# Kernel optimization log

Hardware: AMD Instinct MI355X
Metric: run time of the kernel (lower is better)

The kernel has to match this reference:

```python
import math
import jax, jax.numpy as jnp
import numpy as np

S = 64.0
M = 0.5
C = 1.5
K = 16
EPS = 1e-6
IN = 128
OUT = 10000
B = 1024


def _l2norm(x, axis):
    # matches torch.nn.functional.normalize (eps=1e-12)
    n = jnp.linalg.norm(x, axis=axis, keepdims=True)
    return x / jnp.maximum(n, 1e-12)


def setup_inputs() -> dict:
    key = jax.random.key(0)
    k1, k2, k3, k4 = jax.random.split(key, 4)
    inp = jax.random.normal(k1, (B, IN), dtype=jnp.float32)
    factor = jax.random.uniform(k2, (B, 1), dtype=jnp.float32)
    label = jax.random.randint(k3, (B,), 0, OUT)
    # xavier_uniform over (k, in, out): fan_in=IN, fan_out=OUT (last two dims)
    limit = math.sqrt(6.0 / (IN + OUT))
    weight = jax.random.uniform(k4, (K, IN, OUT), dtype=jnp.float32, minval=-limit, maxval=limit)
    return {"input": inp, "factor": factor, "label": label, "weight": weight}


def reference(input, factor, label, weight):
    # disguise-adaptive margin: (B,1)
    func_a = jnp.power(C, factor / 12.0) * M
    threshold = math.pi - func_a  # (B,1)

    xn = _l2norm(input, axis=1)          # (B, IN)
    wn = _l2norm(weight, axis=1)         # (K, IN, OUT), normalized along IN

    # batched sub-center matmul then max over sub-centers k
    cos_all = jnp.einsum('bf,kfo->kbo', xn, wn)   # (K, B, OUT)
    cos_theta = jnp.max(cos_all, axis=0)          # (B, OUT)

    theta = jnp.arccos(jnp.clip(cos_theta, -1.0 + EPS, 1.0 - EPS))
    one_hot = jax.nn.one_hot(label, OUT, dtype=theta.dtype)  # (B, OUT)
    selected = jnp.where(theta > threshold, jnp.zeros_like(one_hot), one_hot)
    logits = jnp.cos(jnp.where(selected.astype(bool), theta + func_a, theta)) * S

    # cross-entropy (mean reduction)
    logp = jax.nn.log_softmax(logits, axis=-1)
    cls_loss = -jnp.mean(jnp.take_along_axis(logp, label[:, None], axis=1))

    # top-1 accuracy (percent), detached stat
    pred = jnp.argmax(logits, axis=1)
    prec1 = jnp.mean((pred == label).astype(jnp.float32)) * 100.0
    return cls_loss, prec1
```

## Files before the change

kernel.cpp:

```cpp
#include <hip/hip_runtime.h>
#include <hip/hip_bf16.h>
#include <math.h>

#define BB    1024
#define FIN   128
#define NOUT  10000
#define NK    16
#define NBLK  79
#define NPART (NBLK * 2)
#define OPAD  10112
#define LDX   136

typedef __attribute__((ext_vector_type(8))) short short8;
typedef __attribute__((ext_vector_type(4))) float floatx4;

__device__ __forceinline__ unsigned packbf(float a, float b) {
    __hip_bfloat162 h = __float22bfloat162_rn(make_float2(a, b));
    union { __hip_bfloat162 h2; unsigned u; } v;
    v.h2 = h;
    return v.u;
}

__device__ __forceinline__ void async16(const void* g, void* l) {
    __builtin_amdgcn_global_load_lds(
        (const __attribute__((address_space(1))) unsigned int*)g,
        (__attribute__((address_space(3))) unsigned int*)l, 16, 0, 0);
}

__global__ void rowprep(const float* __restrict__ X, const float* __restrict__ factor,
                        float* __restrict__ xinv, float* __restrict__ fa_out,
                        float* __restrict__ thr_out) {
    int b = blockIdx.x;
    int lane = threadIdx.x;
    float v0 = X[b * FIN + lane];
    float v1 = X[b * FIN + 64 + lane];
    float s = v0 * v0 + v1 * v1;
    #pragma unroll
    for (int off = 32; off > 0; off >>= 1) s += __shfl_down(s, off);
    if (lane == 0) {
        float n = sqrtf(s);
        xinv[b] = 1.0f / fmaxf(n, 1e-12f);
        float fa = powf(1.5f, factor[b] * (1.0f / 12.0f)) * 0.5f;
        fa_out[b] = fa;
        thr_out[b] = (float)M_PI - fa;
    }
}

__global__ void wconv(const float* __restrict__ W, unsigned char* __restrict__ Wbf) {
    int t = blockIdx.x * 256 + threadIdx.x;
    int k = t / OPAD;
    int o = t - k * OPAD;
    const bool ok = o < NOUT;
    const float* p = W + (size_t)k * FIN * NOUT + o;
    float v[FIN];
    float s = 0.0f;
    #pragma unroll
    for (int f = 0; f < FIN; f++) {
        float x = ok ? p[(size_t)f * NOUT] : 0.0f;
        v[f] = x;
        s = fmaf(x, x, s);
    }
    float wi = ok ? (1.0f / fmaxf(sqrtf(s), 1e-12f)) : 0.0f;
    unsigned char* dst = Wbf + (size_t)t * 256;
    #pragma unroll
    for (int c = 0; c < 16; c++) {
        uint4 u;
        u.x = packbf(v[c * 8 + 0] * wi, v[c * 8 + 1] * wi);
        u.y = packbf(v[c * 8 + 2] * wi, v[c * 8 + 3] * wi);
        u.z = packbf(v[c * 8 + 4] * wi, v[c * 8 + 5] * wi);
        u.w = packbf(v[c * 8 + 6] * wi, v[c * 8 + 7] * wi);
        *(uint4*)(dst + ((c ^ (o & 15)) * 16)) = u;
    }
}

__global__ __launch_bounds__(256, 2) void gemm_mx(
    const float* __restrict__ X, const unsigned char* __restrict__ Wbf,
    const int* __restrict__ label, const float* __restrict__ xinv,
    float2* __restrict__ partial, float* __restrict__ cosl) {

    __shared__ short lds[32768];

    const int tid  = threadIdx.x;
    const int lane = tid & 63;
    const int w    = tid >> 6;
    const int l15  = lane & 15;
    const int q    = lane >> 4;
    const int wm   = w & 1;
    const int wn   = w >> 1;

    const int id    = blockIdx.x;
    const int group = id >> 6;
    const int sub   = id & 63;
    const int jb    = group * 8 + (sub & 7);
    const int y     = sub >> 3;
    if (jb >= NBLK) return;
    const int r0 = y * 128;
    const int o0 = jb * 128;

    short* xs = lds;
    #pragma unroll
    for (int it = 0; it < 16; it++) {
        int idx = it * 256 + tid;
        int row = idx >> 5;
        int c4  = idx & 31;
        const float4 v = *(const float4*)(X + (size_t)(r0 + row) * FIN + c4 * 4);
        float xi = xinv[r0 + row];
        uint2 p;
        p.x = packbf(v.x * xi, v.y * xi);
        p.y = packbf(v.z * xi, v.w * xi);
        *(uint2*)(xs + row * LDX + c4 * 4) = p;
    }
    __syncthreads();

    short8 af[4][4];
    #pragma unroll
    for (int mt = 0; mt < 4; mt++)
        #pragma unroll
        for (int kk = 0; kk < 4; kk++)
            af[mt][kk] = *(const short8*)(xs + (wm * 64 + mt * 16 + l15) * LDX + kk * 32 + q * 8);
    __syncthreads();

    {
        const unsigned char* g = Wbf + ((size_t)0 * OPAD + o0 + w * 32) * 256 + lane * 16;
        short* d = lds + 0 + w * 4096;
        #pragma unroll
        for (int i = 0; i < 8; i++) async16(g + i * 1024, d + i * 512);
    }

    floatx4 maxv[4][4];
    #pragma unroll
    for (int mt = 0; mt < 4; mt++)
        #pragma unroll
        for (int nt = 0; nt < 4; nt++)
            #pragma unroll
            for (int r = 0; r < 4; r++)
                maxv[mt][nt][r] = -INFINITY;

    for (int k = 0; k < NK; k++) {
        __syncthreads();
        if (k < NK - 1) {
            const unsigned char* g =
                Wbf + ((size_t)(k + 1) * OPAD + o0 + w * 32) * 256 + lane * 16;
            short* d = lds + ((k + 1) & 1) * 16384 + w * 4096;
            #pragma unroll
            for (int i = 0; i < 8; i++) async16(g + i * 1024, d + i * 512);
        }
        const short* wt = lds + (k & 1) * 16384;

        #pragma unroll
        for (int h = 0; h < 2; h++) {
            floatx4 acc[4][2];
            #pragma unroll
            for (int mt = 0; mt < 4; mt++) {
                acc[mt][0] = (floatx4){0.f, 0.f, 0.f, 0.f};
                acc[mt][1] = (floatx4){0.f, 0.f, 0.f, 0.f};
            }
            #pragma unroll
            for (int kk = 0; kk < 4; kk++) {
                short8 bf[2];
                #pragma unroll
                for (int n2 = 0; n2 < 2; n2++) {
                    int col = wn * 64 + (h * 2 + n2) * 16 + l15;
                    int chunk = (kk * 4 + q) ^ l15;
                    bf[n2] = *(const short8*)(wt + col * 128 + chunk * 8);
                }
                #pragma unroll
                for (int mt = 0; mt < 4; mt++) {
                    acc[mt][0] = __builtin_amdgcn_mfma_f32_16x16x32_bf16(af[mt][kk], bf[0], acc[mt][0], 0, 0, 0);
                    acc[mt][1] = __builtin_amdgcn_mfma_f32_16x16x32_bf16(af[mt][kk], bf[1], acc[mt][1], 0, 0, 0);
                }
            }
            #pragma unroll
            for (int mt = 0; mt < 4; mt++)
                #pragma unroll
                for (int n2 = 0; n2 < 2; n2++)
                    #pragma unroll
                    for (int r = 0; r < 4; r++)
                        maxv[mt][h * 2 + n2][r] = fmaxf(maxv[mt][h * 2 + n2][r], acc[mt][n2][r]);
        }
    }

    #pragma unroll
    for (int mt = 0; mt < 4; mt++) {
        #pragma unroll
        for (int rr = 0; rr < 4; rr++) {
            int row = r0 + wm * 64 + mt * 16 + q * 4 + rr;
            int lb = label[row];
            float m = -1e30f, s = 0.f;
            #pragma unroll
            for (int nt = 0; nt < 4; nt++) {
                int o = o0 + wn * 64 + nt * 16 + l15;
                if (o < NOUT) {
                    float c = maxv[mt][nt][rr];
                    if (o == lb) {
                        cosl[row] = c;
                    } else {
                        float l = 64.0f * fminf(fmaxf(c, -1.0f + 1e-6f), 1.0f - 1e-6f);
                        if (l > m) { s = s * __expf(m - l) + 1.0f; m = l; }
                        else       { s += __expf(l - m); }
                    }
                }
            }
            #pragma unroll
            for (int off = 1; off <= 8; off <<= 1) {
                float m2 = __shfl_xor(m, off);
                float s2 = __shfl_xor(s, off);
                float M = fmaxf(m, m2);
                s = s * __expf(m - M) + s2 * __expf(m2 - M);
                m = M;
            }
            if (l15 == 0) partial[(size_t)row * NPART + jb * 2 + wn] = make_float2(m, s);
        }
    }
}

__global__ __launch_bounds__(256, 2) void gemm_stats(
    const float* __restrict__ X, const float* __restrict__ W,
    const int* __restrict__ label, const float* __restrict__ xinv,
    float2* __restrict__ partial, float* __restrict__ cosl) {

    __shared__ short xs[128 * LDX];
    __shared__ short wt[128 * LDX];
    __shared__ float sqs[128][2];

    const int tid  = threadIdx.x;
    const int lane = tid & 63;
    const int w    = tid >> 6;
    const int l15  = lane & 15;
    const int q    = lane >> 4;
    const int wm   = w & 1;
    const int wn   = w >> 1;

    const int id    = blockIdx.x;
    const int group = id >> 6;
    const int sub   = id & 63;
    const int jb    = group * 8 + (sub & 7);
    const int y     = sub >> 3;
    if (jb >= NBLK) return;
    const int r0 = y * 128;
    const int o0 = jb * 128;

    #pragma unroll
    for (int it = 0; it < 16; it++) {
        int idx = it * 256 + tid;
        int row = idx >> 5;
        int c4  = idx & 31;
        const float4 v = *(const float4*)(X + (size_t)(r0 + row) * FIN + c4 * 4);
        uint2 p;
        p.x = packbf(v.x, v.y);
        p.y = packbf(v.z, v.w);
        *(uint2*)(xs + row * LDX + c4 * 4) = p;
    }

    const int st_o = (w & 1) * 64 + lane;
    const int st_f = (w >> 1) * 64;
    const int st_h = w >> 1;
    const int go   = o0 + st_o;
    const bool ov  = go < NOUT;

    float rw[64];
    {
        const float* Wp = W + (size_t)st_f * NOUT + go;
        #pragma unroll
        for (int g = 0; g < 16; g++)
            #pragma unroll
            for (int c = 0; c < 4; c++)
                rw[g * 4 + c] = ov ? Wp[(size_t)(g * 4 + c) * NOUT] : 0.0f;
    }
    __syncthreads();

    short8 af[4][4];
    #pragma unroll
    for (int mt = 0; mt < 4; mt++)
        #pragma unroll
        for (int kk = 0; kk < 4; kk++)
            af[mt][kk] = *(const short8*)(xs + (wm * 64 + mt * 16 + l15) * LDX + kk * 32 + q * 8);

    floatx4 maxv[4][4];
    #pragma unroll
    for (int mt = 0; mt < 4; mt++)
        #pragma unroll
        for (int nt = 0; nt < 4; nt++)
            #pragma unroll
            for (int r = 0; r < 4; r++)
                maxv[mt][nt][r] = -INFINITY;

    for (int k = 0; k < NK; k++) {
        float sq = 0.0f;
        uint2 pk[16];
        #pragma unroll
        for (int g = 0; g < 16; g++) {
            float a0 = rw[g * 4 + 0], a1 = rw[g * 4 + 1];
            float a2 = rw[g * 4 + 2], a3 = rw[g * 4 + 3];
            sq = fmaf(a0, a0, sq); sq = fmaf(a1, a1, sq);
            sq = fmaf(a2, a2, sq); sq = fmaf(a3, a3, sq);
            pk[g].x = packbf(a0, a1);
            pk[g].y = packbf(a2, a3);
        }
        __syncthreads();
        #pragma unroll
        for (int g = 0; g < 16; g++)
            *(uint2*)(wt + st_o * LDX + st_f + g * 4) = pk[g];
        sqs[st_o][st_h] = sq;
        __syncthreads();

        if (k < NK - 1) {
            const float* Wn = W + ((size_t)(k + 1) * FIN + st_f) * NOUT + go;
            #pragma unroll
            for (int g = 0; g < 16; g++)
                #pragma unroll
                for (int c = 0; c < 4; c++)
                    rw[g * 4 + c] = ov ? Wn[(size_t)(g * 4 + c) * NOUT] : 0.0f;
        }

        float wv[4];
        #pragma unroll
        for (int nt = 0; nt < 4; nt++) {
            int col = wn * 64 + nt * 16 + l15;
            wv[nt] = 1.0f / fmaxf(sqrtf(sqs[col][0] + sqs[col][1]), 1e-12f);
        }

        #pragma unroll
        for (int h = 0; h < 2; h++) {
            floatx4 acc[4][2];
            #pragma unroll
            for (int mt = 0; mt < 4; mt++) {
                acc[mt][0] = (floatx4){0.f, 0.f, 0.f, 0.f};
                acc[mt][1] = (floatx4){0.f, 0.f, 0.f, 0.f};
            }
            #pragma unroll
            for (int kk = 0; kk < 4; kk++) {
                short8 bf0 = *(const short8*)(wt + (wn * 64 + (h * 2 + 0) * 16 + l15) * LDX + kk * 32 + q * 8);
                short8 bf1 = *(const short8*)(wt + (wn * 64 + (h * 2 + 1) * 16 + l15) * LDX + kk * 32 + q * 8);
                #pragma unroll
                for (int mt = 0; mt < 4; mt++) {
                    acc[mt][0] = __builtin_amdgcn_mfma_f32_16x16x32_bf16(af[mt][kk], bf0, acc[mt][0], 0, 0, 0);
                    acc[mt][1] = __builtin_amdgcn_mfma_f32_16x16x32_bf16(af[mt][kk], bf1, acc[mt][1], 0, 0, 0);
                }
            }
            #pragma unroll
            for (int mt = 0; mt < 4; mt++)
                #pragma unroll
                for (int n2 = 0; n2 < 2; n2++)
                    #pragma unroll
                    for (int r = 0; r < 4; r++)
                        maxv[mt][h * 2 + n2][r] =
                            fmaxf(maxv[mt][h * 2 + n2][r], acc[mt][n2][r] * wv[h * 2 + n2]);
        }
    }

    #pragma unroll
    for (int mt = 0; mt < 4; mt++) {
        #pragma unroll
        for (int rr = 0; rr < 4; rr++) {
            int row = r0 + wm * 64 + mt * 16 + q * 4 + rr;
            float xi = xinv[row];
            int lb = label[row];
            float m = -1e30f, s = 0.f;
            #pragma unroll
            for (int nt = 0; nt < 4; nt++) {
                int o = o0 + wn * 64 + nt * 16 + l15;
                if (o < NOUT) {
                    float c = maxv[mt][nt][rr] * xi;
                    if (o == lb) {
                        cosl[row] = c;
                    } else {
                        float l = 64.0f * fminf(fmaxf(c, -1.0f + 1e-6f), 1.0f - 1e-6f);
                        if (l > m) { s = s * __expf(m - l) + 1.0f; m = l; }
                        else       { s += __expf(l - m); }
                    }
                }
            }
            #pragma unroll
            for (int off = 1; off <= 8; off <<= 1) {
                float m2 = __shfl_xor(m, off);
                float s2 = __shfl_xor(s, off);
                float M = fmaxf(m, m2);
                s = s * __expf(m - M) + s2 * __expf(m2 - M);
                m = M;
            }
            if (l15 == 0) partial[(size_t)row * NPART + jb * 2 + wn] = make_float2(m, s);
        }
    }
}

__global__ void finalize_rows(const float2* __restrict__ partial, const float* __restrict__ cosl,
                              const float* __restrict__ fa, const float* __restrict__ thr,
                              float2* __restrict__ rowres) {
    int w = threadIdx.x >> 6;
    int lane = threadIdx.x & 63;
    int b = blockIdx.x * 4 + w;
    float m = -1e30f, s = 0.0f;
    for (int j = lane; j < NPART; j += 64) {
        float2 p = partial[(size_t)b * NPART + j];
        float M = fmaxf(m, p.x);
        s = s * __expf(m - M) + p.y * __expf(p.x - M);
        m = M;
    }
    #pragma unroll
    for (int off = 1; off < 64; off <<= 1) {
        float m2 = __shfl_xor(m, off);
        float s2 = __shfl_xor(s, off);
        float M = fmaxf(m, m2);
        s = s * __expf(m - M) + s2 * __expf(m2 - M);
        m = M;
    }
    if (lane == 0) {
        float c = fminf(fmaxf(cosl[b], -1.0f + 1e-6f), 1.0f - 1e-6f);
        float theta = acosf(c);
        float ll = (theta > thr[b]) ? 64.0f * c : 64.0f * cosf(theta + fa[b]);
        float M = fmaxf(m, ll);
        float S = s * __expf(m - M) + __expf(ll - M);
        rowres[b] = make_float2(M + logf(S) - ll, (ll > m) ? 100.0f : 0.0f);
    }
}

__global__ void finalize_sum(const float2* __restrict__ rowres, float* __restrict__ out) {
    __shared__ float sl[1024];
    __shared__ float sc[1024];
    int b = threadIdx.x;
    float2 v = rowres[b];
    sl[b] = v.x;
    sc[b] = v.y;
    __syncthreads();
    for (int st = 512; st > 0; st >>= 1) {
        if (b < st) { sl[b] += sl[b + st]; sc[b] += sc[b + st]; }
        __syncthreads();
    }
    if (b == 0) {
        out[0] = sl[0] * (1.0f / 1024.0f);
        out[1] = sc[0] * (1.0f / 1024.0f);
    }
}

extern "C" void kernel_launch(void* const* d_in, const int* in_sizes, int n_in,
                              void* d_out, int out_size, void* d_ws, size_t ws_size,
                              hipStream_t stream) {
    const float* X      = (const float*)d_in[0];
    const float* factor = (const float*)d_in[1];
    const int*   label  = (const int*)d_in[2];
    const float* W      = (const float*)d_in[3];
    float* out = (float*)d_out;
    float* ws  = (float*)d_ws;

    float*  xinv = ws;
    float*  fa   = ws + 1024;
    float*  thr  = ws + 2048;
    float*  cosl = ws + 3072;
    float2* rowres = (float2*)(ws + 4096);
    float2* partial = (float2*)(ws + 6144);
    unsigned char* Wbf = (unsigned char*)d_ws + 2 * 1024 * 1024;

    const size_t need = 2ull * 1024 * 1024 + (size_t)NK * OPAD * 256;

    rowprep<<<BB, 64, 0, stream>>>(X, factor, xinv, fa, thr);
    if (ws_size >= need) {
        wconv<<<(NK * OPAD) / 256, 256, 0, stream>>>(W, Wbf);
        gemm_mx<<<640, 256, 0, stream>>>(X, Wbf, label, xinv, partial, cosl);
    } else {
        gemm_stats<<<640, 256, 0, stream>>>(X, W, label, xinv, partial, cosl);
    }
    finalize_rows<<<BB / 4, 256, 0, stream>>>(partial, cosl, fa, thr, rowres);
    finalize_sum<<<1, BB, 0, stream>>>(rowres, out);
}
```

Baseline: 222.6 us.

## Restage weight conversion through LDS and halve GEMM weight buffers for occupancy

The weight normalization kernel now loads a 128x128 fp32 tile into shared memory with coalesced float4 reads, reduces column norms cooperatively, and writes bf16 rows in a new layout that groups each 128-column strip into two 64-column halves. Each thread previously did a strided per-column read of 128 elements. The GEMM kernel now streams half-strips per step, running 32 pipeline steps with 16 KB double buffers instead of 16 steps with 32 KB buffers. It also reuses the X staging buffer through a union and raises launch bounds to 3 blocks per CU. The goal is better memory coalescing in the conversion and higher GEMM occupancy, at the cost of twice as many barriers per block.

New measurement: 397.0 us. 1.78x slower.

```diff
diff --git a/kernel.cpp b/kernel.cpp
--- a/kernel.cpp
+++ b/kernel.cpp
@@ -5,10 +5,9 @@
 #define BB    1024
 #define FIN   128
 #define NOUT  10000
+#define NBLK  79
 #define NK    16
-#define NBLK  79
 #define NPART (NBLK * 2)
-#define OPAD  10112
 #define LDX   136
 
 typedef __attribute__((ext_vector_type(8))) short short8;
@@ -46,39 +45,78 @@
     }
 }
 
-__global__ void wconv(const float* __restrict__ W, unsigned char* __restrict__ Wbf) {
-    int t = blockIdx.x * 256 + threadIdx.x;
-    int k = t / OPAD;
-    int o = t - k * OPAD;
-    const bool ok = o < NOUT;
-    const float* p = W + (size_t)k * FIN * NOUT + o;
-    float v[FIN];
+__global__ __launch_bounds__(256) void wconv(const float* __restrict__ W,
+                                             unsigned char* __restrict__ Wbf) {
+    __shared__ float xs2[128 * 128];
+    __shared__ float sq2[256];
+    __shared__ float wis[128];
+
+    const int tid = threadIdx.x;
+    const int k = blockIdx.x / NBLK;
+    const int strip = blockIdx.x - k * NBLK;
+    const int o0 = strip * 128;
+
+    #pragma unroll
+    for (int it = 0; it < 16; it++) {
+        int idx = it * 256 + tid;
+        int f = idx >> 5;
+        int c4 = idx & 31;
+        int o = o0 + c4 * 4;
+        float4 v = make_float4(0.f, 0.f, 0.f, 0.f);
+        if (o < NOUT)
+            v = *(const float4*)(W + ((size_t)k * FIN + f) * NOUT + o);
+        *(float4*)(xs2 + f * 128 + c4 * 4) = v;
+    }
+    __syncthreads();
+
+    const int col = tid & 127;
+    const int half = tid >> 7;
     float s = 0.0f;
-    #pragma unroll
-    for (int f = 0; f < FIN; f++) {
-        float x = ok ? p[(size_t)f * NOUT] : 0.0f;
-        v[f] = x;
+    #pragma unroll 8
+    for (int f2 = 0; f2 < 64; f2++) {
+        float x = xs2[(half * 64 + f2) * 128 + col];
         s = fmaf(x, x, s);
     }
-    float wi = ok ? (1.0f / fmaxf(sqrtf(s), 1e-12f)) : 0.0f;
-    unsigned char* dst = Wbf + (size_t)t * 256;
-    #pragma unroll
-    for (int c = 0; c < 16; c++) {
+    sq2[half * 128 + col] = s;
+    __syncthreads();
+    if (tid < 128)
+        wis[tid] = 1.0f / fmaxf(sqrtf(sq2[tid] + sq2[tid + 128]), 1e-12f);
+    __syncthreads();
+
+    const float wi = wis[col];
+    const int ch = (col >> 5) & 1;
+    const int idx64 = ((col >> 6) << 5) | (col & 31);
+    unsigned char* colbase =
+        Wbf + ((((size_t)k * 2 + ch) * NBLK + strip) * 64 + idx64) * 256;
+    #pragma unroll
+    for (int tcl = 0; tcl < 8; tcl++) {
+        int tc = half * 8 + tcl;
+        float v0 = xs2[(tc * 8 + 0) * 128 + col] * wi;
+        float v1 = xs2[(tc * 8 + 1) * 128 + col] * wi;
+        float v2 = xs2[(tc * 8 + 2) * 128 + col] * wi;
+        float v3 = xs2[(tc * 8 + 3) * 128 + col] * wi;
+        float v4 = xs2[(tc * 8 + 4) * 128 + col] * wi;
+        float v5 = xs2[(tc * 8 + 5) * 128 + col] * wi;
+        float v6 = xs2[(tc * 8 + 6) * 128 + col] * wi;
+        float v7 = xs2[(tc * 8 + 7) * 128 + col] * wi;
         uint4 u;
-        u.x = packbf(v[c * 8 + 0] * wi, v[c * 8 + 1] * wi);
-        u.y = packbf(v[c * 8 + 2] * wi, v[c * 8 + 3] * wi);
-        u.z = packbf(v[c * 8 + 4] * wi, v[c * 8 + 5] * wi);
-        u.w = packbf(v[c * 8 + 6] * wi, v[c * 8 + 7] * wi);
-        *(uint4*)(dst + ((c ^ (o & 15)) * 16)) = u;
-    }
-}
-
-__global__ __launch_bounds__(256, 2) void gemm_mx(
+        u.x = packbf(v0, v1);
+        u.y = packbf(v2, v3);
+        u.z = packbf(v4, v5);
+        u.w = packbf(v6, v7);
+        *(uint4*)(colbase + ((tc ^ (col & 15)) * 16)) = u;
+    }
+}
+
+__global__ __launch_bounds__(256, 3) void gemm_mx(
     const float* __restrict__ X, const unsigned char* __restrict__ Wbf,
     const int* __restrict__ label, const float* __restrict__ xinv,
     float2* __restrict__ partial, float* __restrict__ cosl) {
 
-    __shared__ short lds[32768];
+    __shared__ union {
+        short xs[128 * LDX];
+        short bb[2][8192];
+    } u;
 
     const int tid  = threadIdx.x;
     const int lane = tid & 63;
@@ -95,9 +133,7 @@
     const int y     = sub >> 3;
     if (jb >= NBLK) return;
     const int r0 = y * 128;
-    const int o0 = jb * 128;
-
-    short* xs = lds;
+
     #pragma unroll
     for (int it = 0; it < 16; it++) {
         int idx = it * 256 + tid;
@@ -108,7 +144,7 @@
         uint2 p;
         p.x = packbf(v.x * xi, v.y * xi);
         p.y = packbf(v.z * xi, v.w * xi);
-        *(uint2*)(xs + row * LDX + c4 * 4) = p;
+        *(uint2*)(u.xs + row * LDX + c4 * 4) = p;
     }
     __syncthreads();
 
@@ -117,15 +153,18 @@
     for (int mt = 0; mt < 4; mt++)
         #pragma unroll
         for (int kk = 0; kk < 4; kk++)
-            af[mt][kk] = *(const short8*)(xs + (wm * 64 + mt * 16 + l15) * LDX + kk * 32 + q * 8);
-    __syncthreads();
-
-    {
-        const unsigned char* g = Wbf + ((size_t)0 * OPAD + o0 + w * 32) * 256 + lane * 16;
-        short* d = lds + 0 + w * 4096;
-        #pragma unroll
-        for (int i = 0; i < 8; i++) async16(g + i * 1024, d + i * 512);
-    }
+            af[mt][kk] = *(const short8*)(u.xs + (wm * 64 + mt * 16 + l15) * LDX + kk * 32 + q * 8);
+    __syncthreads();
+
+    auto issue = [&](int ck) {
+        const unsigned char* g = Wbf + ((size_t)ck * NBLK + jb) * 16384
+                                 + (size_t)(w * 4) * 1024 + (size_t)lane * 16;
+        short* d = u.bb[ck & 1] + w * 2048;
+        #pragma unroll
+        for (int i = 0; i < 4; i++) async16(g + i * 1024, d + i * 512);
+    };
+
+    issue(0);
 
     floatx4 maxv[4][4];
     #pragma unroll
@@ -136,50 +175,35 @@
             for (int r = 0; r < 4; r++)
                 maxv[mt][nt][r] = -INFINITY;
 
-    for (int k = 0; k < NK; k++) {
+    for (int ck = 0; ck < 2 * NK; ck++) {
         __syncthreads();
-        if (k < NK - 1) {
-            const unsigned char* g =
-                Wbf + ((size_t)(k + 1) * OPAD + o0 + w * 32) * 256 + lane * 16;
-            short* d = lds + ((k + 1) & 1) * 16384 + w * 4096;
-            #pragma unroll
-            for (int i = 0; i < 8; i++) async16(g + i * 1024, d + i * 512);
-        }
-        const short* wt = lds + (k & 1) * 16384;
-
-        #pragma unroll
-        for (int h = 0; h < 2; h++) {
-            floatx4 acc[4][2];
-            #pragma unroll
-            for (int mt = 0; mt < 4; mt++) {
-                acc[mt][0] = (floatx4){0.f, 0.f, 0.f, 0.f};
-                acc[mt][1] = (floatx4){0.f, 0.f, 0.f, 0.f};
-            }
+        if (ck < 2 * NK - 1) issue(ck + 1);
+        const short* wt = u.bb[ck & 1];
+        const int ch = ck & 1;
+
+        #pragma unroll
+        for (int n2 = 0; n2 < 2; n2++) {
+            const int bidx = wn * 32 + n2 * 16 + l15;
+            floatx4 acc[4];
+            #pragma unroll
+            for (int mt = 0; mt < 4; mt++) acc[mt] = (floatx4){0.f, 0.f, 0.f, 0.f};
             #pragma unroll
             for (int kk = 0; kk < 4; kk++) {
-                short8 bf[2];
+                short8 bf = *(const short8*)(wt + bidx * 128 + (((kk * 4 + q) ^ l15) * 8));
                 #pragma unroll
-                for (int n2 = 0; n2 < 2; n2++) {
-                    int col = wn * 64 + (h * 2 + n2) * 16 + l15;
-                    int chunk = (kk * 4 + q) ^ l15;
-                    bf[n2] = *(const short8*)(wt + col * 128 + chunk * 8);
-                }
-                #pragma unroll
-                for (int mt = 0; mt < 4; mt++) {
-                    acc[mt][0] = __builtin_amdgcn_mfma_f32_16x16x32_bf16(af[mt][kk], bf[0], acc[mt][0], 0, 0, 0);
-                    acc[mt][1] = __builtin_amdgcn_mfma_f32_16x16x32_bf16(af[mt][kk], bf[1], acc[mt][1], 0, 0, 0);
-                }
-            }
+                for (int mt = 0; mt < 4; mt++)
+                    acc[mt] = __builtin_amdgcn_mfma_f32_16x16x32_bf16(af[mt][kk], bf, acc[mt], 0, 0, 0);
+            }
+            const int nt = ch * 2 + n2;
             #pragma unroll
             for (int mt = 0; mt < 4; mt++)
                 #pragma unroll
-                for (int n2 = 0; n2 < 2; n2++)
-                    #pragma unroll
-                    for (int r = 0; r < 4; r++)
-                        maxv[mt][h * 2 + n2][r] = fmaxf(maxv[mt][h * 2 + n2][r], acc[mt][n2][r]);
-        }
-    }
-
+                for (int r = 0; r < 4; r++)
+                    maxv[mt][nt][r] = fmaxf(maxv[mt][nt][r], acc[mt][r]);
+        }
+    }
+
+    const int o0 = jb * 128;
     #pragma unroll
     for (int mt = 0; mt < 4; mt++) {
         #pragma unroll
@@ -451,11 +475,12 @@
     float2* partial = (float2*)(ws + 6144);
     unsigned char* Wbf = (unsigned char*)d_ws + 2 * 1024 * 1024;
 
-    const size_t need = 2ull * 1024 * 1024 + (size_t)NK * OPAD * 256;
+    const size_t wbf_bytes = (size_t)NK * 2 * NBLK * 64 * 256;
+    const size_t need = 2ull * 1024 * 1024 + wbf_bytes;
 
     rowprep<<<BB, 64, 0, stream>>>(X, factor, xinv, fa, thr);
     if (ws_size >= need) {
-        wconv<<<(NK * OPAD) / 256, 256, 0, stream>>>(W, Wbf);
+        wconv<<<NK * NBLK, 256, 0, stream>>>(W, Wbf);
         gemm_mx<<<640, 256, 0, stream>>>(X, Wbf, label, xinv, partial, cosl);
     } else {
         gemm_stats<<<640, 256, 0, stream>>>(X, W, label, xinv, partial, cosl);
```
